# Performance work log

Hardware: AMD Instinct MI355X
Metric: run time of the kernel (lower is better)

The kernel has to match this reference:

```python
import jax, jax.numpy as jnp
import numpy as np

B = 4            # number of scenes (equal-size segments; offset = [M,2M,3M,4M])
K_NEAR = 16
K_FAR = 32
K_SMOOTH = 8
T_LOC = 0.1
T_CON = 0.5
BN_EPS = 1e-5


def setup_inputs() -> dict:
    key = jax.random.key(0)
    ks = jax.random.split(key, 8)
    N, C, H, O = 32768, 6, 64, 1
    coords = jax.random.uniform(ks[0], (N, 3), jnp.float32) * 2.0 - 1.0
    feat = jax.random.normal(ks[1], (N, C), jnp.float32)
    return {
        'feat': feat,
        'coords': coords,
        'W1': jax.random.normal(ks[2], (C, H), jnp.float32) * 0.1,
        'b1': jnp.zeros((H,), jnp.float32),
        'g1': jnp.ones((H,), jnp.float32),
        'be1': jnp.zeros((H,), jnp.float32),
        'W2': jax.random.normal(ks[3], (H, H), jnp.float32) * 0.1,
        'b2': jnp.zeros((H,), jnp.float32),
        'g2': jnp.ones((H,), jnp.float32),
        'be2': jnp.zeros((H,), jnp.float32),
        'W3': jax.random.normal(ks[4], (H, O), jnp.float32) * 0.1,
        'b3': jnp.zeros((O,), jnp.float32),
    }


def _bn_train(x, g, b):
    # BatchNorm1d in train mode: biased batch statistics
    mu = x.mean(axis=0)
    var = x.var(axis=0)
    return g * (x - mu) * jax.lax.rsqrt(var + BN_EPS) + b


def _knn_per_scene(c):
    # c: [M,3] -> [M,K_FAR] sorted nearest-neighbor indices (self first)
    sq = jnp.sum(c * c, axis=-1)                       # [M]
    d2 = sq[:, None] + sq[None, :] - 2.0 * (c @ c.T)   # [M,M] GEMM-based
    return jax.lax.top_k(-d2, K_FAR)[1]                # [M,K_FAR]


def _forward(feat, coords, W1, b1, g1, be1, W2, b2, g2, be2, W3, b3):
    N = feat.shape[0]
    M = N // B
    # ---- PointSorter MLP -> ordering scores in (0,1) ----
    h = jax.nn.gelu(_bn_train(feat @ W1 + b1, g1, be1), approximate=False)
    h = jax.nn.gelu(_bn_train(h @ W2 + b2, g2, be2), approximate=False)
    scores = jax.nn.sigmoid(h @ W3 + b3)               # [N, num_orders]
    s = scores.mean(axis=1, keepdims=True)             # [N,1] (scores_mean)
    # ---- single fused KNN (k=32); slice for k=16 (near) and k=8 (smooth) ----
    cb = coords.reshape(B, M, 3)
    idx = jax.vmap(_knn_per_scene)(cb)                 # [B,M,K_FAR] local
    idx = (idx + (jnp.arange(B) * M)[:, None, None]).reshape(N, K_FAR)
    idx_near = idx[:, :K_NEAR]
    idx_far = idx[:, K_NEAR:]
    idx_sm = idx[:, :K_SMOOTH]
    # ---- locality: neighbors should have similar scores ----
    sd = jnp.abs(s[:, None, :] - s[idx_near])[..., 0]          # [N,16]
    diff = coords[:, None, :] - coords[idx_near]               # [N,16,3]
    d = jnp.sqrt(jnp.maximum(jnp.sum(diff * diff, axis=2), 1e-24))
    w = jnp.exp(-d / T_LOC)
    loss_loc = jnp.sum(w * sd * sd) / jnp.maximum(jnp.sum(w), 1e-8)
    # ---- contrastive: far points should have different scores ----
    sim_pos = 1.0 - jnp.abs(s[:, None, :] - s[idx_near])       # [N,16,1]
    sim_neg = 1.0 - jnp.abs(s[:, None, :] - s[idx_far])        # [N,16,1]
    loss_pos = -jnp.mean(jnp.log(jax.nn.sigmoid(sim_pos / T_CON) + 1e-8))
    loss_neg = -jnp.mean(jnp.log(1.0 - jax.nn.sigmoid(sim_neg / T_CON) + 1e-8))
    loss_con = loss_pos + loss_neg
    # ---- smoothness: score close to mean of 8-NN scores ----
    nmean = s[idx_sm].mean(axis=1)                             # [N,1]
    loss_sm = jnp.mean((s - nmean) ** 2)
    return 1.0 * loss_loc + 0.5 * loss_con + 0.2 * loss_sm


def reference(feat, coords, W1, b1, g1, be1, W2, b2, g2, be2, W3, b3):
    return _forward(feat, coords, W1, b1, g1, be1, W2, b2, g2, be2, W3, b3)
```

## Files before the change

kernel.cpp:

```cpp
#include <hip/hip_runtime.h>

typedef unsigned long long u64;
typedef unsigned int u32;
typedef unsigned short u16;

#define N_PTS 32768
#define M_PTS 8192
#define C_IN 6
#define H_DIM 64

#define G 6
#define NCELL 216
#define NCELL_T 864
#define CW (1.0f/3.0f)

#define NBLK 256
#define KTGT 48.0f

#define TL0 0.0494f
#define TL1 0.0740f
#define TL2 0.1110f
#define TL3 0.1736f
#define TL4 0.2600f
#define TL5 0.4000f


__device__ __forceinline__ float gelu_exact(float x) {
    return 0.5f * x * (1.0f + erff(x * 0.70710678118654752f));
}
__device__ __forceinline__ float sigmoidf_(float x) {
    return 1.0f / (1.0f + expf(-x));
}
__device__ __forceinline__ u64 u64min_(u64 a, u64 b) { return a < b ? a : b; }
__device__ __forceinline__ u64 u64max_(u64 a, u64 b) { return a < b ? b : a; }

__device__ __forceinline__ u64 bitonic_sort64(u64 key, int lane) {
    #pragma unroll
    for (int k = 2; k <= 64; k <<= 1) {
        #pragma unroll
        for (int j = k >> 1; j; j >>= 1) {
            u64 pk = __shfl_xor(key, j, 64);
            bool up = ((lane & k) == 0);
            bool tmin = (((lane & j) == 0) == up);
            key = tmin ? u64min_(key, pk) : u64max_(key, pk);
        }
    }
    return key;
}

__global__ __launch_bounds__(256) void kA(const float* __restrict__ feat,
        const float* __restrict__ coords, const float* __restrict__ W1,
        const float* __restrict__ b1, u32* __restrict__ gcount,
        u16* __restrict__ pcell, float* __restrict__ stats1) {
    __shared__ float red[512];
    int t = threadIdx.x, bid = blockIdx.x;
    if (bid < 128) {
        int n = bid * 256 + t;
        float x = coords[n*3], y = coords[n*3+1], z = coords[n*3+2];
        int cx = min(G-1, max(0, (int)floorf((x + 1.0f) * 3.0f)));
        int cy = min(G-1, max(0, (int)floorf((y + 1.0f) * 3.0f)));
        int cz = min(G-1, max(0, (int)floorf((z + 1.0f) * 3.0f)));
        int gcid = (n >> 13) * NCELL + (cz*G + cy)*G + cx;
        pcell[n] = (u16)gcid;
        atomicAdd(&gcount[gcid], 1u);
    }
    int c = t & 63, w = t >> 6;
    float w1c[C_IN];
    #pragma unroll
    for (int k = 0; k < C_IN; ++k) w1c[k] = W1[k*H_DIM + c];
    float bias = b1[c];
    float s1 = 0.f, s2 = 0.f;
    #pragma unroll 1
    for (int n = bid*8 + w*2; n < N_PTS; n += NBLK*8) {
        const float* fa = feat + n*C_IN;
        const float* fb = feat + (n+1)*C_IN;
        float ha = bias, hb = bias;
        #pragma unroll
        for (int k = 0; k < C_IN; ++k) {
            ha = fmaf(fa[k], w1c[k], ha);
            hb = fmaf(fb[k], w1c[k], hb);
        }
        s1 += ha + hb;
        s2 = fmaf(ha, ha, s2); s2 = fmaf(hb, hb, s2);
    }
    red[w*64 + c] = s1;
    red[256 + w*64 + c] = s2;
    __syncthreads();
    if (t < 64) {
        float a = red[t] + red[64+t] + red[128+t] + red[192+t];
        float b = red[256+t] + red[320+t] + red[384+t] + red[448+t];
        atomicAdd(&stats1[t], a);
        atomicAdd(&stats1[64+t], b);
    }
}

__global__ __launch_bounds__(256) void kB(const float* __restrict__ feat,
        const float* __restrict__ W1, const float* __restrict__ b1,
        const float* __restrict__ stats1, const float* __restrict__ g1,
        const float* __restrict__ be1, const float* __restrict__ W2,
        const float* __restrict__ b2, const u32* __restrict__ gcount,
        u32* __restrict__ cellstart, u32* __restrict__ cellptr,
        float* __restrict__ stats2) {
    __shared__ float red[512];
    __shared__ u32 sc[256];
    int t = threadIdx.x, bid = blockIdx.x;
    if (bid == 0) {
        u32 loc[4]; u32 s = 0;
        #pragma unroll
        for (int j = 0; j < 4; ++j) {
            int idx = t*4 + j;
            loc[j] = (idx < NCELL_T) ? gcount[idx] : 0u;
            s += loc[j];
        }
        sc[t] = s;
        __syncthreads();
        for (int off = 1; off < 256; off <<= 1) {
            u32 v = sc[t];
            if (t >= off) v += sc[t-off];
            __syncthreads();
            sc[t] = v;
            __syncthreads();
        }
        u32 run = sc[t] - s;
        #pragma unroll
        for (int j = 0; j < 4; ++j) {
            int idx = t*4 + j;
            if (idx < NCELL_T) { cellstart[idx] = run; cellptr[idx] = run; }
            run += loc[j];
        }
        if (t == 255) cellstart[NCELL_T] = sc[255];
        __syncthreads();
    }
    int c = t & 63, w = t >> 6;
    float w2c[H_DIM];
    #pragma unroll
    for (int k = 0; k < H_DIM; ++k) w2c[k] = W2[k*H_DIM + c];
    float w1c[C_IN];
    #pragma unroll
    for (int k = 0; k < C_IN; ++k) w1c[k] = W1[k*H_DIM + c];
    float mean1 = stats1[c] * (1.0f/N_PTS);
    float var1  = stats1[64+c] * (1.0f/N_PTS) - mean1*mean1;
    float sc1 = g1[c] * rsqrtf(var1 + 1e-5f);
    float sh1 = be1[c] - mean1*sc1;
    float bias1 = b1[c], bias2 = b2[c];
    float s1 = 0.f, s2 = 0.f;
    #pragma unroll 1
    for (int n = bid*8 + w*2; n < N_PTS; n += NBLK*8) {
        const float* fa = feat + n*C_IN;
        const float* fb = feat + (n+1)*C_IN;
        float ha = bias1, hb = bias1;
        #pragma unroll
        for (int k = 0; k < C_IN; ++k) {
            ha = fmaf(fa[k], w1c[k], ha);
            hb = fmaf(fb[k], w1c[k], hb);
        }
        float aa = gelu_exact(fmaf(sc1, ha, sh1));
        float ab = gelu_exact(fmaf(sc1, hb, sh1));
        float h2a = bias2, h2b = bias2;
        #pragma unroll
        for (int k = 0; k < H_DIM; ++k) {
            h2a = fmaf(__shfl(aa, k, 64), w2c[k], h2a);
            h2b = fmaf(__shfl(ab, k, 64), w2c[k], h2b);
        }
        s1 += h2a + h2b;
        s2 = fmaf(h2a, h2a, s2); s2 = fmaf(h2b, h2b, s2);
    }
    red[w*64 + c] = s1;
    red[256 + w*64 + c] = s2;
    __syncthreads();
    if (t < 64) {
        float a = red[t] + red[64+t] + red[128+t] + red[192+t];
        float b = red[256+t] + red[320+t] + red[384+t] + red[448+t];
        atomicAdd(&stats2[t], a);
        atomicAdd(&stats2[64+t], b);
    }
}

__global__ __launch_bounds__(256) void kC(const float* __restrict__ feat,
        const float* __restrict__ coords,
        const float* __restrict__ W1, const float* __restrict__ b1,
        const float* __restrict__ stats1, const float* __restrict__ g1,
        const float* __restrict__ be1, const float* __restrict__ W2,
        const float* __restrict__ b2, const float* __restrict__ stats2,
        const float* __restrict__ g2v, const float* __restrict__ be2,
        const float* __restrict__ W3, const float* __restrict__ b3,
        const u16* __restrict__ pcell, u32* __restrict__ cellptr,
        float4* __restrict__ P4s, u16* __restrict__ meta16,
        float* __restrict__ S) {
    int t = threadIdx.x, bid = blockIdx.x;
    if (bid < 128) {
        int n = bid * 256 + t;
        float x = coords[n*3], y = coords[n*3+1], z = coords[n*3+2];
        float sq = fmaf(x, x, fmaf(y, y, z*z));
        u32 pos = atomicAdd(&cellptr[pcell[n]], 1u);
        P4s[pos] = make_float4(x, y, z, sq);
        meta16[pos] = (u16)(n & (M_PTS-1));
    }
    int c = t & 63, w = t >> 6;
    float w2c[H_DIM];
    #pragma unroll
    for (int k = 0; k < H_DIM; ++k) w2c[k] = W2[k*H_DIM + c];
    float w1c[C_IN];
    #pragma unroll
    for (int k = 0; k < C_IN; ++k) w1c[k] = W1[k*H_DIM + c];
    float mean1 = stats1[c] * (1.0f/N_PTS);
    float var1  = stats1[64+c] * (1.0f/N_PTS) - mean1*mean1;
    float sc1 = g1[c] * rsqrtf(var1 + 1e-5f);
    float sh1 = be1[c] - mean1*sc1;
    float mean2 = stats2[c] * (1.0f/N_PTS);
    float var2  = stats2[64+c] * (1.0f/N_PTS) - mean2*mean2;
    float sc2 = g2v[c] * rsqrtf(var2 + 1e-5f);
    float sh2 = be2[c] - mean2*sc2;
    float bias1 = b1[c], bias2 = b2[c], w3 = W3[c], bb = b3[0];
    #pragma unroll 1
    for (int n = bid*8 + w*2; n < N_PTS; n += NBLK*8) {
        const float* fa = feat + n*C_IN;
        const float* fb = feat + (n+1)*C_IN;
        float ha = bias1, hb = bias1;
        #pragma unroll
        for (int k = 0; k < C_IN; ++k) {
            ha = fmaf(fa[k], w1c[k], ha);
            hb = fmaf(fb[k], w1c[k], hb);
        }
        float aa = gelu_exact(fmaf(sc1, ha, sh1));
        float ab = gelu_exact(fmaf(sc1, hb, sh1));
        float h2a = bias2, h2b = bias2;
        #pragma unroll
        for (int k = 0; k < H_DIM; ++k) {
            h2a = fmaf(__shfl(aa, k, 64), w2c[k], h2a);
            h2b = fmaf(__shfl(ab, k, 64), w2c[k], h2b);
        }
        float a2a = gelu_exact(fmaf(sc2, h2a, sh2));
        float a2b = gelu_exact(fmaf(sc2, h2b, sh2));
        float va = a2a * w3, vb = a2b * w3;
        #pragma unroll
        for (int m = 32; m; m >>= 1) {
            va += __shfl_xor(va, m, 64);
            vb += __shfl_xor(vb, m, 64);
        }
        if (c == 0) {
            S[n] = sigmoidf_(va + bb);
            S[n+1] = sigmoidf_(vb + bb);
        }
    }
}

__global__ __launch_bounds__(256) void kD(const float4* __restrict__ P4s,
        const u16* __restrict__ meta16, const u32* __restrict__ cellstart,
        const float* __restrict__ S, double* __restrict__ accum,
        u32* __restrict__ donecnt, float* __restrict__ out) {
    __shared__ u64 wavebuf[4][128];
    __shared__ int runsb[16], runse[16];
    __shared__ int nruns_s;
    __shared__ u32 flistB[64];
    __shared__ u32 flnB;
    __shared__ u32 cnt6[6];
    __shared__ u32 ovcnt;
    __shared__ float smacc;
    __shared__ double lred[4][5];

    int t = threadIdx.x, bid = blockIdx.x;
    int lane = t & 63, w = t >> 6;
    u64 lmask = (1ull << lane) - 1ull;
    int scene = bid / NCELL;
    int cid = bid - scene*NCELL;
    int cx = cid % G, cy = (cid / G) % G, cz = cid / (G*G);
    int sbase = scene * M_PTS;

    int ccrd[3] = {cx, cy, cz};
    bool wall[3]; int Wn = 0;
    #pragma unroll
    for (int d = 0; d < 3; ++d) { wall[d] = (ccrd[d] == 0 || ccrd[d] == G-1); Wn += wall[d]; }
    int lo[3], hi[3];
    #pragma unroll
    for (int d = 0; d < 3; ++d) {
        if (Wn >= 2 && !wall[d]) { lo[d] = min(max(ccrd[d]-2, 0), G-5); hi[d] = lo[d]+4; }
        else                     { lo[d] = min(max(ccrd[d]-1, 0), G-3); hi[d] = lo[d]+2; }
    }
    float lof[3], hif[3]; bool lw[3], hw[3];
    #pragma unroll
    for (int d = 0; d < 3; ++d) {
        lof[d] = -1.0f + lo[d]*CW; hif[d] = -1.0f + (hi[d]+1)*CW;
        lw[d] = (lo[d] == 0); hw[d] = (hi[d] == G-1);
    }
    if (t == 0) {
        int nr = 0;
        int nx = hi[0]-lo[0]+1;
        for (int z = lo[2]; z <= hi[2]; ++z)
            for (int y = lo[1]; y <= hi[1]; ++y) {
                int bc = scene*NCELL + (z*G + y)*G + lo[0];
                runsb[nr] = (int)cellstart[bc];
                runse[nr] = (int)cellstart[bc + nx];
                ++nr;
            }
        nruns_s = nr;
        flnB = 0;
    }
    int gcid = scene*NCELL + cid;
    int qstart = (int)cellstart[gcid];
    int qn = (int)cellstart[gcid+1] - qstart;
    __syncthreads();
    int nruns = nruns_s;

    double anum=0.0, aden=0.0, aslp=0.0, asln=0.0, asmo=0.0;

    for (int pq = w; pq < qn; pq += 4) {
        int qglob = qstart + pq;
        float4 qc = P4s[qglob];
        float qsq = qc.w;
        float qd[3] = {qc.x, qc.y, qc.z};
        float cov = 1e9f;
        #pragma unroll
        for (int d = 0; d < 3; ++d) {
            if (!lw[d]) cov = fminf(cov, qd[d] - lof[d]);
            if (!hw[d]) cov = fminf(cov, hif[d] - qd[d]);
        }
        float g2 = cov*cov;
        float axx = fminf(qc.x+1.f, 1.f-qc.x);
        float ayy = fminf(qc.y+1.f, 1.f-qc.y);
        float azz = fminf(qc.z+1.f, 1.f-qc.z);
        float r = 0.224f;
        #pragma unroll
        for (int it = 0; it < 3; ++it) {
            float ir = 1.0f / r;
            float ux = fminf(axx*ir, 1.f), uy = fminf(ayy*ir, 1.f), uz = fminf(azz*ir, 1.f);
            float fx = 0.25f*(2.f + 3.f*ux - ux*ux*ux);
            float fy = 0.25f*(2.f + 3.f*uy - uy*uy*uy);
            float fz = 0.25f*(2.f + 3.f*uz - uz*uz*uz);
            r = cbrtf(KTGT / (4289.32f * fx * fy * fz));
        }
        float taup = fminf(r*r, g2) - qsq;

        u32 base = 0;
        for (int rr = 0; rr < nruns; ++rr) {
            int ve = runse[rr];
            #pragma unroll 1
            for (int v0 = runsb[rr]; v0 < ve; v0 += 64) {
                int v = v0 + lane;
                bool pred = false; u64 key = 0;
                if (v < ve) {
                    float4 pp = P4s[v];
                    float dot = fmaf(qc.x, pp.x, fmaf(qc.y, pp.y, qc.z*pp.z));
                    float e2 = fmaf(-2.0f, dot, pp.w);
                    if (e2 < taup) {
                        pred = true;
                        float d2 = fmaxf(e2 + qsq, 0.0f);
                        key = ((u64)__float_as_uint(d2) << 13) | (u64)meta16[v];
                    }
                }
                u64 mask = __ballot(pred);
                if (pred) {
                    u32 pos = base + (u32)__popcll(mask & lmask);
                    if (pos < 128u) wavebuf[w][pos] = key;
                }
                base += (u32)__popcll(mask);
            }
        }

        if (base < 32u || base > 128u) {
            if (lane == 0) {
                u32 idx = atomicAdd(&flnB, 1u);
                if (idx < 64u) flistB[idx] = (u32)qglob;
            }
            continue;
        }

        u32 M = base;
        u64 k0 = (lane < (int)min(M, 64u)) ? wavebuf[w][lane] : ~0ull;
        k0 = bitonic_sort64(k0, lane);
        if (M > 64u) {
            u64 k1 = (lane < (int)(M - 64u)) ? wavebuf[w][64 + lane] : ~0ull;
            k1 = bitonic_sort64(k1, lane);
            u64 pk = __shfl(k1, 63 - lane, 64);
            u64 lo2 = u64min_(k0, pk);
            #pragma unroll
            for (int j = 32; j; j >>= 1) {
                u64 pj = __shfl_xor(lo2, j, 64);
                lo2 = ((lane & j) == 0) ? u64min_(lo2, pj) : u64max_(lo2, pj);
            }
            k0 = lo2;
        }

        float si = S[sbase + (int)meta16[qglob]];
        float smsum = 0.f;
        if (lane < 32) {
            float d2 = __uint_as_float((u32)(k0 >> 13));
            u32 jo = (u32)(k0 & 0x1FFFu);
            float sj = S[sbase + (int)jo];
            float sd = fabsf(si - sj);
            float sim = 1.0f - sd;
            if (lane < 16) {
                float d = sqrtf(fmaxf(d2, 1e-24f));
                float wgt = expf(-10.0f*d);
                anum += (double)(wgt*sd*sd);
                aden += (double)wgt;
                aslp += (double)logf(sigmoidf_(2.0f*sim) + 1e-8f);
                if (lane < 8) smsum += sj;
            } else {
                asln += (double)logf(sigmoidf_(-2.0f*sim) + 1e-8f);
            }
        }
        #pragma unroll
        for (int m = 32; m; m >>= 1) smsum += __shfl_xor(smsum, m, 64);
        if (lane == 0) {
            float dd = si - smsum*0.125f;
            asmo += (double)(dd*dd);
        }
    }
    __syncthreads();

    int nf = min((int)flnB, 64);
    u64* ovbuf = &wavebuf[0][0];
    for (int f = 0; f < nf; ++f) {
        int fqg = (int)flistB[f];
        float4 fqc = P4s[fqg];
        float fsq = fqc.w;
        float fcov = 1e9f;
        float fqd[3] = {fqc.x, fqc.y, fqc.z};
        #pragma unroll
        for (int d = 0; d < 3; ++d) {
            if (!lw[d]) fcov = fminf(fcov, fqd[d] - lof[d]);
            if (!hw[d]) fcov = fminf(fcov, hif[d] - fqd[d]);
        }
        float fg2 = fcov*fcov;
        if (t < 6) cnt6[t] = 0;
        if (t == 0) { ovcnt = 0; smacc = 0.f; }
        __syncthreads();
        u32 c0=0,c1=0,c2=0,c3=0,c4=0,c5=0;
        for (int rr = 0; rr < nruns; ++rr) {
            for (int v = runsb[rr] + t; v < runse[rr]; v += 256) {
                float4 pp = P4s[v];
                float dot = fmaf(fqc.x, pp.x, fmaf(fqc.y, pp.y, fqc.z*pp.z));
                float e2 = fmaf(-2.0f, dot, pp.w);
                c0 += (e2 < TL0-fsq); c1 += (e2 < TL1-fsq); c2 += (e2 < TL2-fsq);
                c3 += (e2 < TL3-fsq); c4 += (e2 < TL4-fsq); c5 += (e2 < TL5-fsq);
            }
        }
        #pragma unroll
        for (int m = 32; m; m >>= 1) {
            c0 += __shfl_xor(c0, m, 64); c1 += __shfl_xor(c1, m, 64);
            c2 += __shfl_xor(c2, m, 64); c3 += __shfl_xor(c3, m, 64);
            c4 += __shfl_xor(c4, m, 64); c5 += __shfl_xor(c5, m, 64);
        }
        if (lane == 0) {
            atomicAdd(&cnt6[0], c0); atomicAdd(&cnt6[1], c1);
            atomicAdd(&cnt6[2], c2); atomicAdd(&cnt6[3], c3);
            atomicAdd(&cnt6[4], c4); atomicAdd(&cnt6[5], c5);
        }
        __syncthreads();
        float tau = TL2;
        if (TL3 <= fg2) tau = TL3;
        if (TL4 <= fg2) tau = TL4;
        if (TL5 <= fg2) tau = TL5;
        if      (cnt6[0] >= 32u) tau = TL0;
        else if (cnt6[1] >= 32u) tau = TL1;
        else if (cnt6[2] >= 32u) tau = TL2;
        else if (TL3 <= fg2 && cnt6[3] >= 32u) tau = TL3;
        else if (TL4 <= fg2 && cnt6[4] >= 32u) tau = TL4;
        else if (TL5 <= fg2 && cnt6[5] >= 32u) tau = TL5;
        float ftp = tau - fsq;
        for (int rr = 0; rr < nruns; ++rr) {
            for (int v = runsb[rr] + t; v < runse[rr]; v += 256) {
                float4 pp = P4s[v];
                float dot = fmaf(fqc.x, pp.x, fmaf(fqc.y, pp.y, fqc.z*pp.z));
                float e2 = fmaf(-2.0f, dot, pp.w);
                if (e2 < ftp) {
                    float d2 = fmaxf(e2 + fsq, 0.0f);
                    u64 key = ((u64)__float_as_uint(d2) << 13) | (u64)meta16[v];
                    u32 pos = atomicAdd(&ovcnt, 1u);
                    if (pos < 512u) ovbuf[pos] = key;
                }
            }
        }
        __syncthreads();
        u32 Mf = min(ovcnt, 512u);
        float fsi = S[sbase + (int)meta16[fqg]];
        for (int i = t; i < (int)Mf; i += 256) {
            u64 mykey = ovbuf[i];
            u32 rank = 0;
            for (u32 j = 0; j < Mf; ++j) rank += (ovbuf[j] < mykey);
            if (rank < 32u) {
                float d2 = __uint_as_float((u32)(mykey >> 13));
                u32 jo = (u32)(mykey & 0x1FFFu);
                float sj = S[sbase + (int)jo];
                float sd = fabsf(fsi - sj);
                float sim = 1.0f - sd;
                if (rank < 16u) {
                    float d = sqrtf(fmaxf(d2, 1e-24f));
                    float wgt = expf(-10.0f*d);
                    anum += (double)(wgt*sd*sd);
                    aden += (double)wgt;
                    aslp += (double)logf(sigmoidf_(2.0f*sim) + 1e-8f);
                    if (rank < 8u) atomicAdd(&smacc, sj);
                } else {
                    asln += (double)logf(sigmoidf_(-2.0f*sim) + 1e-8f);
                }
            }
        }
        __syncthreads();
        if (t == 0) {
            float dd = fsi - smacc*0.125f;
            asmo += (double)(dd*dd);
        }
        __syncthreads();
    }

    double v[5] = {anum, aden, aslp, asln, asmo};
    #pragma unroll
    for (int k = 0; k < 5; ++k) {
        for (int m = 32; m; m >>= 1) v[k] += __shfl_xor(v[k], m, 64);
    }
    if (lane == 0) {
        #pragma unroll
        for (int k = 0; k < 5; ++k) lred[w][k] = v[k];
    }
    __syncthreads();
    if (t == 0) {
        #pragma unroll
        for (int k = 0; k < 5; ++k)
            atomicAdd(&accum[k], lred[0][k] + lred[1][k] + lred[2][k] + lred[3][k]);
        __threadfence();
        u32 old = atomicAdd(donecnt, 1u);
        if (old == (u32)(NCELL_T - 1)) {
            double a0 = atomicAdd(&accum[0], 0.0);
            double a1 = atomicAdd(&accum[1], 0.0);
            double a2 = atomicAdd(&accum[2], 0.0);
            double a3 = atomicAdd(&accum[3], 0.0);
            double a4 = atomicAdd(&accum[4], 0.0);
            double loss_loc = a0 / fmax(a1, 1e-8);
            double inv = 1.0 / ((double)N_PTS * 16.0);
            double loss_con = -(a2 * inv) - (a3 * inv);
            double loss_sm = a4 / (double)N_PTS;
            out[0] = (float)(loss_loc + 0.5*loss_con + 0.2*loss_sm);
        }
    }
}

extern "C" void kernel_launch(void* const* d_in, const int* in_sizes, int n_in,
                              void* d_out, int out_size, void* d_ws, size_t ws_size,
                              hipStream_t stream) {
    const float* feat   = (const float*)d_in[0];
    const float* coords = (const float*)d_in[1];
    const float* W1 = (const float*)d_in[2];
    const float* b1 = (const float*)d_in[3];
    const float* g1 = (const float*)d_in[4];
    const float* be1= (const float*)d_in[5];
    const float* g2 = (const float*)d_in[8];
    const float* W2 = (const float*)d_in[6];
    const float* b2 = (const float*)d_in[7];
    const float* be2= (const float*)d_in[9];
    const float* W3 = (const float*)d_in[10];
    const float* b3 = (const float*)d_in[11];
    char* ws = (char*)d_ws;

    float* stats1   = (float*)(ws);
    float* stats2   = (float*)(ws + 512);
    u32* gcount     = (u32*)(ws + 1024);
    double* accum   = (double*)(ws + 4480);
    u32* donecnt    = (u32*)(ws + 4520);
    u32* cellstart  = (u32*)(ws + 4544);
    u32* cellptr    = (u32*)(ws + 8008);
    float* S        = (float*)(ws + 11472);
    float4* P4s     = (float4*)(ws + 142544);
    u16* meta16     = (u16*)(ws + 666832);
    u16* pcell      = (u16*)(ws + 732368);

    hipMemsetAsync(d_ws, 0, 4544, stream);

    hipLaunchKernelGGL(kA, dim3(NBLK), dim3(256), 0, stream,
                       feat, coords, W1, b1, gcount, pcell, stats1);
    hipLaunchKernelGGL(kB, dim3(NBLK), dim3(256), 0, stream,
                       feat, W1, b1, stats1, g1, be1, W2, b2,
                       gcount, cellstart, cellptr, stats2);
    hipLaunchKernelGGL(kC, dim3(NBLK), dim3(256), 0, stream,
                       feat, coords, W1, b1, stats1, g1, be1, W2, b2,
                       stats2, g2, be2, W3, b3, pcell, cellptr, P4s, meta16, S);
    hipLaunchKernelGGL(kD, dim3(NCELL_T), dim3(256), 0, stream,
                       P4s, meta16, cellstart, S, accum, donecnt, (float*)d_out);
}
```

Measured before the change: 346.4 us.

## Batch four queries per wave and split each cell across two blocks

The kNN kernel now has each wave process a group of four queries together. Every candidate point loaded from the neighbouring cells is tested against all four queries, which cuts global loads of candidates per query. The grid is doubled so each cell's queries are divided between two blocks, which raises parallelism on the GPU. In exchange, register pressure and shared-memory use go up (wavebuf is four times larger), and the fallback list is now per half-block.

```diff
diff --git a/kernel.cpp b/kernel.cpp
--- a/kernel.cpp
+++ b/kernel.cpp
@@ -15,6 +15,7 @@
 #define CW (1.0f/3.0f)
 
 #define NBLK 256
+#define QG 4
 #define KTGT 48.0f
 
 #define TL0 0.0494f
@@ -249,7 +250,7 @@
         const u16* __restrict__ meta16, const u32* __restrict__ cellstart,
         const float* __restrict__ S, double* __restrict__ accum,
         u32* __restrict__ donecnt, float* __restrict__ out) {
-    __shared__ u64 wavebuf[4][128];
+    __shared__ u64 wavebuf[4][QG][128];
     __shared__ int runsb[16], runse[16];
     __shared__ int nruns_s;
     __shared__ u32 flistB[64];
@@ -262,8 +263,9 @@
     int t = threadIdx.x, bid = blockIdx.x;
     int lane = t & 63, w = t >> 6;
     u64 lmask = (1ull << lane) - 1ull;
-    int scene = bid / NCELL;
-    int cid = bid - scene*NCELL;
+    int cell = bid >> 1, half = bid & 1;
+    int scene = cell / NCELL;
+    int cid = cell - scene*NCELL;
     int cx = cid % G, cy = (cid / G) % G, cz = cid / (G*G);
     int sbase = scene * M_PTS;
 
@@ -301,116 +303,142 @@
     int qn = (int)cellstart[gcid+1] - qstart;
     __syncthreads();
     int nruns = nruns_s;
+    int hq = (qn + 1) >> 1;
+    int hqs = qstart + half * hq;
+    int hqn = qn - half * hq; if (hqn > hq) hqn = hq; if (hqn < 0) hqn = 0;
 
     double anum=0.0, aden=0.0, aslp=0.0, asln=0.0, asmo=0.0;
 
-    for (int pq = w; pq < qn; pq += 4) {
-        int qglob = qstart + pq;
-        float4 qc = P4s[qglob];
-        float qsq = qc.w;
-        float qd[3] = {qc.x, qc.y, qc.z};
-        float cov = 1e9f;
-        #pragma unroll
-        for (int d = 0; d < 3; ++d) {
-            if (!lw[d]) cov = fminf(cov, qd[d] - lof[d]);
-            if (!hw[d]) cov = fminf(cov, hif[d] - qd[d]);
-        }
-        float g2 = cov*cov;
-        float axx = fminf(qc.x+1.f, 1.f-qc.x);
-        float ayy = fminf(qc.y+1.f, 1.f-qc.y);
-        float azz = fminf(qc.z+1.f, 1.f-qc.z);
-        float r = 0.224f;
-        #pragma unroll
-        for (int it = 0; it < 3; ++it) {
-            float ir = 1.0f / r;
-            float ux = fminf(axx*ir, 1.f), uy = fminf(ayy*ir, 1.f), uz = fminf(azz*ir, 1.f);
-            float fx = 0.25f*(2.f + 3.f*ux - ux*ux*ux);
-            float fy = 0.25f*(2.f + 3.f*uy - uy*uy*uy);
-            float fz = 0.25f*(2.f + 3.f*uz - uz*uz*uz);
-            r = cbrtf(KTGT / (4289.32f * fx * fy * fz));
-        }
-        float taup = fminf(r*r, g2) - qsq;
-
-        u32 base = 0;
+    for (int g0 = w*QG; g0 < hqn; g0 += 4*QG) {
+        int jcount = min(QG, hqn - g0);
+        int qb = hqs + g0;
+        float qx[QG], qy[QG], qz[QG], qs[QG], tp[QG];
+        u32 baseq[QG];
+        #pragma unroll
+        for (int j = 0; j < QG; ++j) {
+            int qg = qb + min(j, jcount-1);
+            float4 qc = P4s[qg];
+            qx[j]=qc.x; qy[j]=qc.y; qz[j]=qc.z; qs[j]=qc.w;
+            float cov = 1e9f;
+            float qdv[3] = {qc.x, qc.y, qc.z};
+            #pragma unroll
+            for (int d = 0; d < 3; ++d) {
+                if (!lw[d]) cov = fminf(cov, qdv[d] - lof[d]);
+                if (!hw[d]) cov = fminf(cov, hif[d] - qdv[d]);
+            }
+            float g2 = cov*cov;
+            float axx = fminf(qc.x+1.f, 1.f-qc.x);
+            float ayy = fminf(qc.y+1.f, 1.f-qc.y);
+            float azz = fminf(qc.z+1.f, 1.f-qc.z);
+            float r = 0.224f;
+            #pragma unroll
+            for (int it = 0; it < 3; ++it) {
+                float ir = 1.0f / r;
+                float ux = fminf(axx*ir, 1.f), uy = fminf(ayy*ir, 1.f), uz = fminf(azz*ir, 1.f);
+                float fx = 0.25f*(2.f + 3.f*ux - ux*ux*ux);
+                float fy = 0.25f*(2.f + 3.f*uy - uy*uy*uy);
+                float fz = 0.25f*(2.f + 3.f*uz - uz*uz*uz);
+                r = cbrtf(KTGT / (4289.32f * fx * fy * fz));
+            }
+            tp[j] = (j < jcount) ? (fminf(r*r, g2) - qc.w) : -1e30f;
+            baseq[j] = 0;
+        }
+
         for (int rr = 0; rr < nruns; ++rr) {
             int ve = runse[rr];
-            #pragma unroll 1
-            for (int v0 = runsb[rr]; v0 < ve; v0 += 64) {
-                int v = v0 + lane;
-                bool pred = false; u64 key = 0;
-                if (v < ve) {
-                    float4 pp = P4s[v];
-                    float dot = fmaf(qc.x, pp.x, fmaf(qc.y, pp.y, qc.z*pp.z));
-                    float e2 = fmaf(-2.0f, dot, pp.w);
-                    if (e2 < taup) {
-                        pred = true;
-                        float d2 = fmaxf(e2 + qsq, 0.0f);
-                        key = ((u64)__float_as_uint(d2) << 13) | (u64)meta16[v];
+            for (int v0 = runsb[rr]; v0 < ve; v0 += 128) {
+                int vA = v0 + lane, vB = v0 + 64 + lane;
+                bool okA = vA < ve, okB = vB < ve;
+                float4 pA = make_float4(0.f,0.f,0.f,1e30f);
+                float4 pB = make_float4(0.f,0.f,0.f,1e30f);
+                u32 mA = 0, mB = 0;
+                if (okA) { pA = P4s[vA]; mA = (u32)meta16[vA]; }
+                if (okB) { pB = P4s[vB]; mB = (u32)meta16[vB]; }
+                #pragma unroll
+                for (int j = 0; j < QG; ++j) {
+                    float dotA = fmaf(qx[j], pA.x, fmaf(qy[j], pA.y, qz[j]*pA.z));
+                    float e2A = fmaf(-2.0f, dotA, pA.w);
+                    bool prA = okA && (e2A < tp[j]);
+                    u64 mkA = __ballot(prA);
+                    if (prA) {
+                        float d2 = fmaxf(e2A + qs[j], 0.0f);
+                        u64 key = ((u64)__float_as_uint(d2) << 13) | (u64)mA;
+                        u32 pos = baseq[j] + (u32)__popcll(mkA & lmask);
+                        if (pos < 128u) wavebuf[w][j][pos] = key;
                     }
+                    baseq[j] += (u32)__popcll(mkA);
+                    float dotB = fmaf(qx[j], pB.x, fmaf(qy[j], pB.y, qz[j]*pB.z));
+                    float e2B = fmaf(-2.0f, dotB, pB.w);
+                    bool prB = okB && (e2B < tp[j]);
+                    u64 mkB = __ballot(prB);
+                    if (prB) {
+                        float d2 = fmaxf(e2B + qs[j], 0.0f);
+                        u64 key = ((u64)__float_as_uint(d2) << 13) | (u64)mB;
+                        u32 pos = baseq[j] + (u32)__popcll(mkB & lmask);
+                        if (pos < 128u) wavebuf[w][j][pos] = key;
+                    }
+                    baseq[j] += (u32)__popcll(mkB);
                 }
-                u64 mask = __ballot(pred);
-                if (pred) {
-                    u32 pos = base + (u32)__popcll(mask & lmask);
-                    if (pos < 128u) wavebuf[w][pos] = key;
+            }
+        }
+
+        #pragma unroll
+        for (int j = 0; j < QG; ++j) {
+            if (j >= jcount) continue;
+            int qg = qb + j;
+            u32 M = baseq[j];
+            if (M < 32u || M > 128u) {
+                if (lane == 0) {
+                    u32 idx = atomicAdd(&flnB, 1u);
+                    if (idx < 64u) flistB[idx] = (u32)qg;
                 }
-                base += (u32)__popcll(mask);
-            }
-        }
-
-        if (base < 32u || base > 128u) {
+                continue;
+            }
+            u64 k0 = (lane < (int)min(M, 64u)) ? wavebuf[w][j][lane] : ~0ull;
+            k0 = bitonic_sort64(k0, lane);
+            if (M > 64u) {
+                u64 k1 = (lane < (int)(M - 64u)) ? wavebuf[w][j][64 + lane] : ~0ull;
+                k1 = bitonic_sort64(k1, lane);
+                u64 pk = __shfl(k1, 63 - lane, 64);
+                u64 lo2 = u64min_(k0, pk);
+                #pragma unroll
+                for (int jj = 32; jj; jj >>= 1) {
+                    u64 pj = __shfl_xor(lo2, jj, 64);
+                    lo2 = ((lane & jj) == 0) ? u64min_(lo2, pj) : u64max_(lo2, pj);
+                }
+                k0 = lo2;
+            }
+            float si = S[sbase + (int)meta16[qg]];
+            float smsum = 0.f;
+            if (lane < 32) {
+                float d2 = __uint_as_float((u32)(k0 >> 13));
+                u32 jo = (u32)(k0 & 0x1FFFu);
+                float sj = S[sbase + (int)jo];
+                float sd = fabsf(si - sj);
+                float sim = 1.0f - sd;
+                if (lane < 16) {
+                    float d = sqrtf(fmaxf(d2, 1e-24f));
+                    float wgt = expf(-10.0f*d);
+                    anum += (double)(wgt*sd*sd);
+                    aden += (double)wgt;
+                    aslp += (double)logf(sigmoidf_(2.0f*sim) + 1e-8f);
+                    if (lane < 8) smsum += sj;
+                } else {
+                    asln += (double)logf(sigmoidf_(-2.0f*sim) + 1e-8f);
+                }
+            }
+            #pragma unroll
+            for (int m = 32; m; m >>= 1) smsum += __shfl_xor(smsum, m, 64);
             if (lane == 0) {
-                u32 idx = atomicAdd(&flnB, 1u);
-                if (idx < 64u) flistB[idx] = (u32)qglob;
-            }
-            continue;
-        }
-
-        u32 M = base;
-        u64 k0 = (lane < (int)min(M, 64u)) ? wavebuf[w][lane] : ~0ull;
-        k0 = bitonic_sort64(k0, lane);
-        if (M > 64u) {
-            u64 k1 = (lane < (int)(M - 64u)) ? wavebuf[w][64 + lane] : ~0ull;
-            k1 = bitonic_sort64(k1, lane);
-            u64 pk = __shfl(k1, 63 - lane, 64);
-            u64 lo2 = u64min_(k0, pk);
-            #pragma unroll
-            for (int j = 32; j; j >>= 1) {
-                u64 pj = __shfl_xor(lo2, j, 64);
-                lo2 = ((lane & j) == 0) ? u64min_(lo2, pj) : u64max_(lo2, pj);
-            }
-            k0 = lo2;
-        }
-
-        float si = S[sbase + (int)meta16[qglob]];
-        float smsum = 0.f;
-        if (lane < 32) {
-            float d2 = __uint_as_float((u32)(k0 >> 13));
-            u32 jo = (u32)(k0 & 0x1FFFu);
-            float sj = S[sbase + (int)jo];
-            float sd = fabsf(si - sj);
-            float sim = 1.0f - sd;
-            if (lane < 16) {
-                float d = sqrtf(fmaxf(d2, 1e-24f));
-                float wgt = expf(-10.0f*d);
-                anum += (double)(wgt*sd*sd);
-                aden += (double)wgt;
-                aslp += (double)logf(sigmoidf_(2.0f*sim) + 1e-8f);
-                if (lane < 8) smsum += sj;
-            } else {
-                asln += (double)logf(sigmoidf_(-2.0f*sim) + 1e-8f);
-            }
-        }
-        #pragma unroll
-        for (int m = 32; m; m >>= 1) smsum += __shfl_xor(smsum, m, 64);
-        if (lane == 0) {
-            float dd = si - smsum*0.125f;
-            asmo += (double)(dd*dd);
+                float dd = si - smsum*0.125f;
+                asmo += (double)(dd*dd);
+            }
         }
     }
     __syncthreads();
 
     int nf = min((int)flnB, 64);
-    u64* ovbuf = &wavebuf[0][0];
+    u64* ovbuf = &wavebuf[0][0][0];
     for (int f = 0; f < nf; ++f) {
         int fqg = (int)flistB[f];
         float4 fqc = P4s[fqg];
@@ -478,7 +506,7 @@
         for (int i = t; i < (int)Mf; i += 256) {
             u64 mykey = ovbuf[i];
             u32 rank = 0;
-            for (u32 j = 0; j < Mf; ++j) rank += (ovbuf[j] < mykey);
+            for (u32 jj = 0; jj < Mf; ++jj) rank += (ovbuf[jj] < mykey);
             if (rank < 32u) {
                 float d2 = __uint_as_float((u32)(mykey >> 13));
                 u32 jo = (u32)(mykey & 0x1FFFu);
@@ -521,7 +549,7 @@
             atomicAdd(&accum[k], lred[0][k] + lred[1][k] + lred[2][k] + lred[3][k]);
         __threadfence();
         u32 old = atomicAdd(donecnt, 1u);
-        if (old == (u32)(NCELL_T - 1)) {
+        if (old == (u32)(2*NCELL_T - 1)) {
             double a0 = atomicAdd(&accum[0], 0.0);
             double a1 = atomicAdd(&accum[1], 0.0);
             double a2 = atomicAdd(&accum[2], 0.0);
@@ -545,9 +573,9 @@
     const float* b1 = (const float*)d_in[3];
     const float* g1 = (const float*)d_in[4];
     const float* be1= (const float*)d_in[5];
-    const float* g2 = (const float*)d_in[8];
     const float* W2 = (const float*)d_in[6];
     const float* b2 = (const float*)d_in[7];
+    const float* g2 = (const float*)d_in[8];
     const float* be2= (const float*)d_in[9];
     const float* W3 = (const float*)d_in[10];
     const float* b3 = (const float*)d_in[11];
@@ -575,6 +603,6 @@
     hipLaunchKernelGGL(kC, dim3(NBLK), dim3(256), 0, stream,
                        feat, coords, W1, b1, stats1, g1, be1, W2, b2,
                        stats2, g2, be2, W3, b3, pcell, cellptr, P4s, meta16, S);
-    hipLaunchKernelGGL(kD, dim3(NCELL_T), dim3(256), 0, stream,
+    hipLaunchKernelGGL(kD, dim3(2*NCELL_T), dim3(256), 0, stream,
                        P4s, meta16, cellstart, S, accum, donecnt, (float*)d_out);
 }
```

New measurement: 325.6 us. 1.06x faster.
